# Kernel optimization log

Measured on AMD Instinct MI355X. Metric: run time of the kernel, lower is better.

Reference implementation:

```python
import jax, jax.numpy as jnp
import numpy as np

N, E, G = 64, 128, 4
D0, ED = 9, 4
H1, H2, H3 = 2000, 500, 100
F1, F2, F3 = 1000, 100, 50


def setup_inputs() -> dict:
    key = jax.random.key(0)
    ks = iter(jax.random.split(key, 32))

    def p(shape, s=0.02):
        return (jax.random.normal(next(ks), shape, jnp.float32) * s)

    inp = {
        "x": jax.random.normal(next(ks), (N, D0), jnp.float32),
        "edge_index": jax.random.randint(next(ks), (2, E), 0, N),
        "edge_attr": jax.random.normal(next(ks), (E, ED), jnp.float32),
        "batch": jnp.sort(jax.random.randint(next(ks), (N,), 0, G)),
        # NNConv layer 1: edge MLP Linear(ED, D0*H1), root weight, bias
        "We1": p((ED, D0 * H1)), "be1": p((D0 * H1,)),
        "root1": p((D0, H1)), "b1": p((H1,)),
        # NNConv layer 2
        "We2": p((ED, H1 * H2)), "be2": p((H1 * H2,)),
        "root2": p((H1, H2)), "b2": p((H2,)),
        # NNConv layer 3
        "We3": p((ED, H2 * H3)), "be3": p((H2 * H3,)),
        "root3": p((H2, H3)), "b3": p((H3,)),
        # FCN head
        "W1": p((H3, F1)), "c1": p((F1,)),
        "W2": p((F1, F2)), "c2": p((F2,)),
        "W3": p((F2, F3)), "c3": p((F3,)),
        "W4": p((F3, 1)), "c4": p((1,)),
    }
    return inp


def _nnconv(x, src, dst, edge_attr, We, be, root, b):
    # edge-conditioned weights: [E, in, out]
    in_dim = x.shape[1]
    w = (edge_attr @ We + be).reshape(edge_attr.shape[0], in_dim, -1)
    # gather source feats, per-edge matmul, scatter-add to targets
    msg = jnp.einsum('ei,eio->eo', x[src], w)
    agg = jax.ops.segment_sum(msg, dst, num_segments=x.shape[0])
    return agg + x @ root + b


def reference(x, edge_index, edge_attr, batch,
              We1, be1, root1, b1,
              We2, be2, root2, b2,
              We3, be3, root3, b3,
              W1, c1, W2, c2, W3, c3, W4, c4):
    src, dst = edge_index[0], edge_index[1]
    h = jax.nn.relu(_nnconv(x, src, dst, edge_attr, We1, be1, root1, b1))
    h = jax.nn.relu(_nnconv(h, src, dst, edge_attr, We2, be2, root2, b2))
    h = jax.nn.relu(_nnconv(h, src, dst, edge_attr, We3, be3, root3, b3))
    # sum readout per graph (dropout layers are identity in eval mode)
    g = jax.ops.segment_sum(h, batch, num_segments=G)  # [G, H3]
    g = jax.nn.relu(g @ W1 + c1)
    g = jax.nn.relu(g @ W2 + c2)
    g = jax.nn.relu(g @ W3 + c3)
    out = g @ W4 + c4
    return out.reshape(-1)  # [G]
```

## Files before the change

### kernel.cpp

```cpp
#include <hip/hip_runtime.h>

#define NN 64
#define EE 128
#define GG 4
#define D0 9
#define EDIM 4
#define H1 2000
#define H2 500
#define H3 100
#define FF1 1000
#define FF2 100
#define FF3 50

#define OFF_ACH  0
#define OFF_Y    24576
#define OFF_P1   28032
#define OFF_Q    156032
#define OFF_PART 924032
#define OFF_P2   2524032
#define OFF_PRE3 2556032
#define OFF_F1   2562432
#define OFF_F2   2566432

__device__ __forceinline__ void gl2lds16(const float* g, float* l) {
    __builtin_amdgcn_global_load_lds(
        (const __attribute__((address_space(1))) unsigned int*)g,
        (__attribute__((address_space(3))) unsigned int*)l,
        16, 0, 0);
}

__device__ __forceinline__ float4 ldf4(const float* p) {
    return *(const float4*)p;
}

__device__ __forceinline__ void waitcnt_vm_n(int n) {
    switch (n) {
    case 0: asm volatile("s_waitcnt vmcnt(0)" ::: "memory"); break;
    case 1: asm volatile("s_waitcnt vmcnt(1)" ::: "memory"); break;
    case 2: asm volatile("s_waitcnt vmcnt(2)" ::: "memory"); break;
    case 3: asm volatile("s_waitcnt vmcnt(3)" ::: "memory"); break;
    case 4: asm volatile("s_waitcnt vmcnt(4)" ::: "memory"); break;
    case 5: asm volatile("s_waitcnt vmcnt(5)" ::: "memory"); break;
    default: asm volatile("s_waitcnt vmcnt(6)" ::: "memory"); break;
    }
}
__device__ __forceinline__ void cfence() { asm volatile("" ::: "memory"); }

__global__ __launch_bounds__(256) void k_init(
    const float* __restrict__ x, const int* __restrict__ edge_index,
    const float* __restrict__ edge_attr, const float* __restrict__ c2,
    float* __restrict__ ws)
{
    const int b = blockIdx.x, tid = threadIdx.x;
    if (b == 0) {
        float* A = ws + OFF_ACH;
        for (int i = tid; i < 6 * NN * NN; i += 256) A[i] = 0.f;
        __syncthreads();
        if (tid < EE) {
            int s = edge_index[tid];
            int t = edge_index[EE + tid];
            #pragma unroll
            for (int d = 0; d < 4; ++d)
                atomicAdd(A + d * 4096 + t * 64 + s, edge_attr[tid * 4 + d]);
            atomicAdd(A + 4 * 4096 + t * 64 + s, 1.0f);
        }
        if (tid < NN) A[5 * 4096 + tid * 64 + tid] = 1.0f;
    } else if (b == 1) {
        __shared__ float Ys[NN * 54];
        for (int i = tid; i < NN * 54; i += 256) Ys[i] = 0.f;
        __syncthreads();
        if (tid < EE) {
            int s = edge_index[tid];
            int t = edge_index[EE + tid];
            float ea[4];
            #pragma unroll
            for (int d = 0; d < 4; ++d) ea[d] = edge_attr[tid * 4 + d];
            #pragma unroll
            for (int i = 0; i < D0; ++i) {
                float xv = x[s * D0 + i];
                #pragma unroll
                for (int d = 0; d < 4; ++d)
                    atomicAdd(&Ys[t * 54 + d * 9 + i], ea[d] * xv);
                atomicAdd(&Ys[t * 54 + 36 + i], xv);
            }
        }
        if (tid < NN) {
            #pragma unroll
            for (int i = 0; i < D0; ++i) Ys[tid * 54 + 45 + i] = x[tid * D0 + i];
        }
        __syncthreads();
        for (int i = tid; i < NN * 54; i += 256) ws[OFF_Y + i] = Ys[i];
    } else {
        for (int i = tid; i < GG * FF2; i += 256) ws[OFF_F2 + i] = c2[i % FF2];
    }
}

__global__ __launch_bounds__(256) void k_lin1(
    const float* __restrict__ Yw,
    const float* __restrict__ We1, const float* __restrict__ be1,
    const float* __restrict__ root1, const float* __restrict__ b1,
    float* __restrict__ pre1)
{
    const int tid = threadIdx.x;
    const int tx = tid & 15, ty = tid >> 4;
    const int o0 = blockIdx.x * 64;
    const int w = min(64, H1 - o0);

    __shared__ float Ys[64 * 56];
    __shared__ __align__(16) float Bs[54 * 64];

    for (int i = tid; i < 64 * 54; i += 256) {
        int u = i / 54, r = i - u * 54;
        Ys[u * 56 + r] = Yw[i];
    }
    for (int i = tid; i < 54 * 64; i += 256) {
        int r = i >> 6, c = i & 63;
        int d = r / 9, ii = r - d * 9;
        const float* rowp = ((d < 4) ? (We1 + d * (D0 * H1))
                                     : ((d == 4) ? be1 : root1)) + ii * H1;
        Bs[r * 64 + c] = (c < w) ? rowp[o0 + c] : 0.f;
    }
    __syncthreads();

    float acc[4][4] = {};
    #pragma unroll 6
    for (int r = 0; r < 54; ++r) {
        float a0 = Ys[(ty * 4 + 0) * 56 + r];
        float a1 = Ys[(ty * 4 + 1) * 56 + r];
        float a2 = Ys[(ty * 4 + 2) * 56 + r];
        float a3 = Ys[(ty * 4 + 3) * 56 + r];
        const float4 bv = *(const float4*)&Bs[r * 64 + tx * 4];
        acc[0][0] += a0 * bv.x; acc[0][1] += a0 * bv.y; acc[0][2] += a0 * bv.z; acc[0][3] += a0 * bv.w;
        acc[1][0] += a1 * bv.x; acc[1][1] += a1 * bv.y; acc[1][2] += a1 * bv.z; acc[1][3] += a1 * bv.w;
        acc[2][0] += a2 * bv.x; acc[2][1] += a2 * bv.y; acc[2][2] += a2 * bv.z; acc[2][3] += a2 * bv.w;
        acc[3][0] += a3 * bv.x; acc[3][1] += a3 * bv.y; acc[3][2] += a3 * bv.z; acc[3][3] += a3 * bv.w;
    }
    #pragma unroll
    for (int i = 0; i < 4; ++i) {
        int u = ty * 4 + i;
        #pragma unroll
        for (int jj = 0; jj < 4; ++jj) {
            int j = o0 + tx * 4 + jj;
            if (j < H1) {
                float v = b1[j] + acc[i][jj];
                pre1[u * H1 + j] = v > 0.f ? v : 0.f;
            }
        }
    }
}

template<int Kd, int KTOT, int NKT>
__global__ __launch_bounds__(256) void k_q(
    const float* __restrict__ Ach, const float* __restrict__ P,
    float* __restrict__ Qf)
{
    const int bx = blockIdx.x;
    const int d = bx / NKT, kt = bx % NKT;
    const int k0 = kt * 128;
    const int tid = threadIdx.x;
    const int kq = tid & 31;
    const int rg = tid >> 5;
    const int nf4 = (min(128, Kd - k0) + 3) >> 2;

    __shared__ __align__(16) float Al[64 * 64];
    __shared__ __align__(16) float Pl[64 * 128];

    const float* Ad = Ach + d * 4096;
    for (int i4 = tid; i4 < 1024; i4 += 256)
        *(float4*)&Al[i4 * 4] = ldf4(Ad + i4 * 4);
    for (int i4 = tid; i4 < 64 * 32; i4 += 256) {
        int u = i4 >> 5, c4 = i4 & 31;
        float4 v = {0.f, 0.f, 0.f, 0.f};
        if (c4 < nf4) v = ldf4(P + u * Kd + k0 + c4 * 4);
        *(float4*)&Pl[u * 128 + c4 * 4] = v;
    }
    __syncthreads();

    float acc[8][4] = {};
    #pragma unroll 4
    for (int u4 = 0; u4 < 16; ++u4) {
        float4 pv0 = ldf4(&Pl[(u4 * 4 + 0) * 128 + kq * 4]);
        float4 pv1 = ldf4(&Pl[(u4 * 4 + 1) * 128 + kq * 4]);
        float4 pv2 = ldf4(&Pl[(u4 * 4 + 2) * 128 + kq * 4]);
        float4 pv3 = ldf4(&Pl[(u4 * 4 + 3) * 128 + kq * 4]);
        #pragma unroll
        for (int i = 0; i < 8; ++i) {
            float4 a = ldf4(&Al[(rg * 8 + i) * 64 + u4 * 4]);
            acc[i][0] += a.x * pv0.x + a.y * pv1.x + a.z * pv2.x + a.w * pv3.x;
            acc[i][1] += a.x * pv0.y + a.y * pv1.y + a.z * pv2.y + a.w * pv3.y;
            acc[i][2] += a.x * pv0.z + a.y * pv1.z + a.z * pv2.z + a.w * pv3.z;
            acc[i][3] += a.x * pv0.w + a.y * pv1.w + a.z * pv2.w + a.w * pv3.w;
        }
    }
    const int k = k0 + kq * 4;
    if (k < Kd) {
        #pragma unroll
        for (int i = 0; i < 8; ++i) {
            int r = rg * 8 + i;
            *(float4*)(Qf + r * KTOT + d * Kd + k) =
                make_float4(acc[i][0], acc[i][1], acc[i][2], acc[i][3]);
        }
    }
}

template<int M, int OT, int S, int ITERS, int T1, int T2>
__global__ __launch_bounds__(256) void k_split(
    const float* __restrict__ Qf, const float* __restrict__ We,
    const float* __restrict__ be, const float* __restrict__ root,
    float* __restrict__ part)
{
    constexpr int KC = 20, BN = 32;
    constexpr int KTOT = S * ITERS * KC;
    constexpr int AC = (64 * KC) / 256;
    constexpr int BFL = KC * BN;
    constexpr int BC = (BFL + 255) / 256;
    const int b = blockIdx.x;
    const int s = b % S, ot = b / S;
    const int o0 = ot * BN;
    const int tid = threadIdx.x;
    const int tx = tid & 7, ty = tid >> 3;
    const int wv = tid >> 6, ln = tid & 63;
    const int kbase = s * (KC * ITERS);
    const int nw = ((AC - wv + 3) >> 2) + ((wv < BC) ? ((BC - wv + 3) >> 2) : 0);

    __shared__ __align__(16) float As[2][64 * KC];
    __shared__ __align__(16) float Bs[2][KC * BN];

    auto stage = [&](int bf, int kb) {
        for (int c = wv; c < AC; c += 4) {
            int f = c * 256 + ln * 4;
            int r = f / KC, kkk = f - r * KC;
            gl2lds16(Qf + r * KTOT + kb + kkk, &As[bf][c * 256]);
        }
        for (int c = wv; c < BC; c += 4) {
            int f = c * 256 + ln * 4;
            if (f < BFL) {
                int krow = f / BN, col = f - krow * BN;
                int kg = kb + krow;
                const float* bp = (kg < T1) ? (We + (long long)kg * M)
                                : (kg < T2) ? (be + (long long)(kg - T1) * M)
                                            : (root + (long long)(kg - T2) * M);
                int cc = min(o0 + col, M - 4);
                gl2lds16(bp + cc, &Bs[bf][c * 256]);
            }
        }
    };

    float acc[2][4] = {};
    stage(0, kbase);

    for (int it = 0; it < ITERS; ++it) {
        int npend = 0;
        if (it + 1 < ITERS) { stage((it + 1) & 1, kbase + (it + 1) * KC); npend = nw; }
        waitcnt_vm_n(npend);
        __builtin_amdgcn_s_barrier();
        __builtin_amdgcn_sched_barrier(0);

        const float* Ab = As[it & 1];
        const float* Bb = Bs[it & 1];
        #pragma unroll
        for (int k4 = 0; k4 < KC / 4; ++k4) {
            float4 a0 = ldf4(&Ab[(ty * 2 + 0) * KC + k4 * 4]);
            float4 a1 = ldf4(&Ab[(ty * 2 + 1) * KC + k4 * 4]);
            float4 b0 = ldf4(&Bb[(k4 * 4 + 0) * BN + tx * 4]);
            float4 b1 = ldf4(&Bb[(k4 * 4 + 1) * BN + tx * 4]);
            float4 b2 = ldf4(&Bb[(k4 * 4 + 2) * BN + tx * 4]);
            float4 b3 = ldf4(&Bb[(k4 * 4 + 3) * BN + tx * 4]);
            acc[0][0] += a0.x * b0.x; acc[0][1] += a0.x * b0.y; acc[0][2] += a0.x * b0.z; acc[0][3] += a0.x * b0.w;
            acc[0][0] += a0.y * b1.x; acc[0][1] += a0.y * b1.y; acc[0][2] += a0.y * b1.z; acc[0][3] += a0.y * b1.w;
            acc[0][0] += a0.z * b2.x; acc[0][1] += a0.z * b2.y; acc[0][2] += a0.z * b2.z; acc[0][3] += a0.z * b2.w;
            acc[0][0] += a0.w * b3.x; acc[0][1] += a0.w * b3.y; acc[0][2] += a0.w * b3.z; acc[0][3] += a0.w * b3.w;
            acc[1][0] += a1.x * b0.x; acc[1][1] += a1.x * b0.y; acc[1][2] += a1.x * b0.z; acc[1][3] += a1.x * b0.w;
            acc[1][0] += a1.y * b1.x; acc[1][1] += a1.y * b1.y; acc[1][2] += a1.y * b1.z; acc[1][3] += a1.y * b1.w;
            acc[1][0] += a1.z * b2.x; acc[1][1] += a1.z * b2.y; acc[1][2] += a1.z * b2.z; acc[1][3] += a1.z * b2.w;
            acc[1][0] += a1.w * b3.x; acc[1][1] += a1.w * b3.y; acc[1][2] += a1.w * b3.z; acc[1][3] += a1.w * b3.w;
        }
        cfence();
        __builtin_amdgcn_sched_barrier(0);
        __builtin_amdgcn_s_barrier();
    }

    float* dst = part + s * (64 * M);
    #pragma unroll
    for (int i = 0; i < 2; ++i) {
        int u = ty * 2 + i;
        #pragma unroll
        for (int jj = 0; jj < 4; ++jj) {
            int j = o0 + tx * 4 + jj;
            if (j < M) dst[u * M + j] = acc[i][jj];
        }
    }
}

__global__ __launch_bounds__(256) void k_red2(
    const float* __restrict__ part, const float* __restrict__ b2,
    float* __restrict__ P2)
{
    int i4 = blockIdx.x * 256 + threadIdx.x;
    if (i4 >= (64 * 500) / 4) return;
    int o = (i4 * 4) % 500;
    float4 acc = ldf4(b2 + o);
    #pragma unroll 10
    for (int s = 0; s < 50; ++s) {
        float4 v = ldf4(part + s * 32000 + i4 * 4);
        acc.x += v.x; acc.y += v.y; acc.z += v.z; acc.w += v.w;
    }
    acc.x = fmaxf(acc.x, 0.f); acc.y = fmaxf(acc.y, 0.f);
    acc.z = fmaxf(acc.z, 0.f); acc.w = fmaxf(acc.w, 0.f);
    *(float4*)(P2 + i4 * 4) = acc;
}

__global__ __launch_bounds__(256) void k_red3(
    const float* __restrict__ part, const float* __restrict__ b3,
    float* __restrict__ pre3)
{
    int i4 = blockIdx.x * 256 + threadIdx.x;
    if (i4 >= (64 * 100) / 4) return;
    int o = (i4 * 4) % 100;
    float4 acc = ldf4(b3 + o);
    #pragma unroll 10
    for (int s = 0; s < 50; ++s) {
        float4 v = ldf4(part + s * 6400 + i4 * 4);
        acc.x += v.x; acc.y += v.y; acc.z += v.z; acc.w += v.w;
    }
    *(float4*)(pre3 + i4 * 4) = acc;
}

__global__ __launch_bounds__(256) void k_head1(
    const float* __restrict__ pre3, const int* __restrict__ batch,
    const float* __restrict__ W1, const float* __restrict__ c1,
    float* __restrict__ f1)
{
    const int gi = blockIdx.x >> 4;
    const int jt = blockIdx.x & 15;
    const int o0 = jt * 64;
    const int tid = threadIdx.x;
    __shared__ int   bsh[NN];
    __shared__ float gs[H3];
    __shared__ float red[4 * 64];

    if (tid < NN) bsh[tid] = batch[tid];
    __syncthreads();
    for (int d = tid; d < H3; d += 256) {
        float acc = 0.f;
        #pragma unroll
        for (int v = 0; v < NN; ++v) {
            float h = pre3[v * H3 + d];
            h = h > 0.f ? h : 0.f;
            acc += (bsh[v] == gi) ? h : 0.f;
        }
        gs[d] = acc;
    }
    __syncthreads();
    const int jj = tid & 63, kq = tid >> 6;
    const int oc = min(o0 + jj, FF1 - 1);
    float p = 0.f;
    #pragma unroll
    for (int k = kq * 25; k < kq * 25 + 25; ++k)
        p += gs[k] * W1[k * FF1 + oc];
    red[kq * 64 + jj] = p;
    __syncthreads();
    if (tid < 64) {
        int o = o0 + tid;
        if (o < FF1) {
            float v = c1[o] + red[tid] + red[64 + tid] + red[128 + tid] + red[192 + tid];
            f1[gi * FF1 + o] = v > 0.f ? v : 0.f;
        }
    }
}

__global__ __launch_bounds__(256) void k_head2(
    const float* __restrict__ f1, const float* __restrict__ W2,
    float* __restrict__ f2)
{
    const int s = blockIdx.x;
    const int k0 = s * 63;
    const int kn = min(63, FF1 - k0);
    const int tid = threadIdx.x;
    __shared__ float f1s[4 * 63];
    for (int i = tid; i < 4 * kn; i += 256) {
        int gi = i / kn, kk = i - gi * kn;
        f1s[gi * 63 + kk] = f1[gi * FF1 + k0 + kk];
    }
    __syncthreads();
    for (int idx = tid; idx < GG * FF2; idx += 256) {
        int gi = idx / FF2, o = idx - gi * FF2;
        float acc = 0.f;
        for (int kk = 0; kk < kn; ++kk)
            acc += f1s[gi * 63 + kk] * W2[(k0 + kk) * FF2 + o];
        atomicAdd(&f2[idx], acc);
    }
}

__global__ __launch_bounds__(256) void k_head3(
    const float* __restrict__ f2, const float* __restrict__ W3,
    const float* __restrict__ c3, const float* __restrict__ W4,
    const float* __restrict__ c4, float* __restrict__ out)
{
    const int tid = threadIdx.x;
    __shared__ float f2s[GG * FF2];
    __shared__ float f3s[GG * FF3];
    for (int i = tid; i < GG * FF2; i += 256) {
        float v = f2[i];
        f2s[i] = v > 0.f ? v : 0.f;
    }
    __syncthreads();
    if (tid < GG * FF3) {
        int gi = tid / FF3, o = tid - gi * FF3;
        float acc = c3[o];
        for (int k = 0; k < FF2; ++k)
            acc += f2s[gi * FF2 + k] * W3[k * FF3 + o];
        f3s[tid] = acc > 0.f ? acc : 0.f;
    }
    __syncthreads();
    if (tid < GG) {
        float acc = c4[0];
        #pragma unroll
        for (int k = 0; k < FF3; ++k) acc += f3s[tid * FF3 + k] * W4[k];
        out[tid] = acc;
    }
}

extern "C" void kernel_launch(void* const* d_in, const int* in_sizes, int n_in,
                              void* d_out, int out_size, void* d_ws, size_t ws_size,
                              hipStream_t stream) {
    const float* x          = (const float*)d_in[0];
    const int*   edge_index = (const int*)  d_in[1];
    const float* edge_attr  = (const float*)d_in[2];
    const int*   batch      = (const int*)  d_in[3];
    const float* We1 = (const float*)d_in[4];
    const float* be1 = (const float*)d_in[5];
    const float* root1 = (const float*)d_in[6];
    const float* b1  = (const float*)d_in[7];
    const float* We2 = (const float*)d_in[8];
    const float* be2 = (const float*)d_in[9];
    const float* root2 = (const float*)d_in[10];
    const float* b2  = (const float*)d_in[11];
    const float* We3 = (const float*)d_in[12];
    const float* be3 = (const float*)d_in[13];
    const float* root3 = (const float*)d_in[14];
    const float* b3  = (const float*)d_in[15];
    const float* W1 = (const float*)d_in[16];
    const float* c1 = (const float*)d_in[17];
    const float* W2 = (const float*)d_in[18];
    const float* c2 = (const float*)d_in[19];
    const float* W3 = (const float*)d_in[20];
    const float* c3 = (const float*)d_in[21];
    const float* W4 = (const float*)d_in[22];
    const float* c4 = (const float*)d_in[23];
    float* ws  = (float*)d_ws;
    float* out = (float*)d_out;

    k_init<<<3, 256, 0, stream>>>(x, edge_index, edge_attr, c2, ws);
    k_lin1<<<32, 256, 0, stream>>>(ws + OFF_Y, We1, be1, root1, b1, ws + OFF_P1);
    k_q<2000, 12000, 16><<<96, 256, 0, stream>>>(ws + OFF_ACH, ws + OFF_P1,
                                                 ws + OFF_Q);
    k_split<500, 16, 50, 12, 8000, 10000><<<800, 256, 0, stream>>>(
        ws + OFF_Q, We2, be2, root2, ws + OFF_PART);
    k_red2<<<32, 256, 0, stream>>>(ws + OFF_PART, b2, ws + OFF_P2);
    k_q<500, 3000, 4><<<24, 256, 0, stream>>>(ws + OFF_ACH, ws + OFF_P2,
                                              ws + OFF_Q);
    k_split<100, 4, 50, 3, 2000, 2500><<<200, 256, 0, stream>>>(
        ws + OFF_Q, We3, be3, root3, ws + OFF_PART);
    k_red3<<<7, 256, 0, stream>>>(ws + OFF_PART, b3, ws + OFF_PRE3);
    k_head1<<<64, 256, 0, stream>>>(ws + OFF_PRE3, batch, W1, c1, ws + OFF_F1);
    k_head2<<<16, 256, 0, stream>>>(ws + OFF_F1, W2, ws + OFF_F2);
    k_head3<<<1, 256, 0, stream>>>(ws + OFF_F2, W3, c3, W4, c4, out);
}
```

Baseline: 216.5 us.

## Fuse init/reduction kernels into consumers and widen split GEMM tile

Removes the separate init, red2, red3 and head2/head3 kernels. Each consumer now rebuilds the adjacency matrices in shared memory, sums the split-K partials on load, or computes the FC head tail in a single block, which cuts the launch count from 11 to 7. The split GEMM tile widens from 32 to 64 output columns with a 4x4 per-thread micro-tile, which halves the grid. The cost is redundant recomputation: adjacency building is repeated in every block, the 50-way partial reduction is repeated in each head1 block, and the single-block head2 no longer spreads its work across blocks.

```diff
diff --git a/kernel.cpp b/kernel.cpp
--- a/kernel.cpp
+++ b/kernel.cpp
@@ -4,7 +4,6 @@
 #define EE 128
 #define GG 4
 #define D0 9
-#define EDIM 4
 #define H1 2000
 #define H2 500
 #define H3 100
@@ -12,15 +11,10 @@
 #define FF2 100
 #define FF3 50
 
-#define OFF_ACH  0
-#define OFF_Y    24576
 #define OFF_P1   28032
 #define OFF_Q    156032
 #define OFF_PART 924032
-#define OFF_P2   2524032
-#define OFF_PRE3 2556032
 #define OFF_F1   2562432
-#define OFF_F2   2566432
 
 __device__ __forceinline__ void gl2lds16(const float* g, float* l) {
     __builtin_amdgcn_global_load_lds(
@@ -36,82 +30,93 @@
 __device__ __forceinline__ void waitcnt_vm_n(int n) {
     switch (n) {
     case 0: asm volatile("s_waitcnt vmcnt(0)" ::: "memory"); break;
-    case 1: asm volatile("s_waitcnt vmcnt(1)" ::: "memory"); break;
     case 2: asm volatile("s_waitcnt vmcnt(2)" ::: "memory"); break;
-    case 3: asm volatile("s_waitcnt vmcnt(3)" ::: "memory"); break;
     case 4: asm volatile("s_waitcnt vmcnt(4)" ::: "memory"); break;
-    case 5: asm volatile("s_waitcnt vmcnt(5)" ::: "memory"); break;
     default: asm volatile("s_waitcnt vmcnt(6)" ::: "memory"); break;
     }
 }
 __device__ __forceinline__ void cfence() { asm volatile("" ::: "memory"); }
 
-__global__ __launch_bounds__(256) void k_init(
+__device__ __forceinline__ void build_Ad(float* Al, int d,
+    const int* __restrict__ ei, const float* __restrict__ ea, int tid)
+{
+    for (int i = tid; i < NN * NN; i += 256) Al[i] = 0.f;
+    __syncthreads();
+    if (d == 5) {
+        if (tid < NN) Al[tid * 64 + tid] = 1.0f;
+    } else if (tid < EE) {
+        int s = ei[tid], t = ei[EE + tid];
+        float v = (d < 4) ? ea[tid * 4 + d] : 1.0f;
+        atomicAdd(&Al[t * 64 + s], v);
+    }
+}
+
+template<int Kd, int KTOT>
+__device__ __forceinline__ void q_compute_store(
+    const float* Al, const float* Pl, float* __restrict__ Qf,
+    int d, int k0, int tid)
+{
+    const int kq = tid & 31, rg = tid >> 5;
+    float acc[8][4] = {};
+    #pragma unroll 4
+    for (int u4 = 0; u4 < 16; ++u4) {
+        float4 pv0 = ldf4(&Pl[(u4 * 4 + 0) * 128 + kq * 4]);
+        float4 pv1 = ldf4(&Pl[(u4 * 4 + 1) * 128 + kq * 4]);
+        float4 pv2 = ldf4(&Pl[(u4 * 4 + 2) * 128 + kq * 4]);
+        float4 pv3 = ldf4(&Pl[(u4 * 4 + 3) * 128 + kq * 4]);
+        #pragma unroll
+        for (int i = 0; i < 8; ++i) {
+            float4 a = ldf4(&Al[(rg * 8 + i) * 64 + u4 * 4]);
+            acc[i][0] += a.x * pv0.x + a.y * pv1.x + a.z * pv2.x + a.w * pv3.x;
+            acc[i][1] += a.x * pv0.y + a.y * pv1.y + a.z * pv2.y + a.w * pv3.y;
+            acc[i][2] += a.x * pv0.z + a.y * pv1.z + a.z * pv2.z + a.w * pv3.z;
+            acc[i][3] += a.x * pv0.w + a.y * pv1.w + a.z * pv2.w + a.w * pv3.w;
+        }
+    }
+    const int k = k0 + kq * 4;
+    if (k < Kd) {
+        #pragma unroll
+        for (int i = 0; i < 8; ++i) {
+            int r = rg * 8 + i;
+            *(float4*)(Qf + r * KTOT + d * Kd + k) =
+                make_float4(acc[i][0], acc[i][1], acc[i][2], acc[i][3]);
+        }
+    }
+}
+
+__global__ __launch_bounds__(256) void k_p1(
     const float* __restrict__ x, const int* __restrict__ edge_index,
-    const float* __restrict__ edge_attr, const float* __restrict__ c2,
-    float* __restrict__ ws)
-{
-    const int b = blockIdx.x, tid = threadIdx.x;
-    if (b == 0) {
-        float* A = ws + OFF_ACH;
-        for (int i = tid; i < 6 * NN * NN; i += 256) A[i] = 0.f;
-        __syncthreads();
-        if (tid < EE) {
-            int s = edge_index[tid];
-            int t = edge_index[EE + tid];
-            #pragma unroll
-            for (int d = 0; d < 4; ++d)
-                atomicAdd(A + d * 4096 + t * 64 + s, edge_attr[tid * 4 + d]);
-            atomicAdd(A + 4 * 4096 + t * 64 + s, 1.0f);
-        }
-        if (tid < NN) A[5 * 4096 + tid * 64 + tid] = 1.0f;
-    } else if (b == 1) {
-        __shared__ float Ys[NN * 54];
-        for (int i = tid; i < NN * 54; i += 256) Ys[i] = 0.f;
-        __syncthreads();
-        if (tid < EE) {
-            int s = edge_index[tid];
-            int t = edge_index[EE + tid];
-            float ea[4];
-            #pragma unroll
-            for (int d = 0; d < 4; ++d) ea[d] = edge_attr[tid * 4 + d];
-            #pragma unroll
-            for (int i = 0; i < D0; ++i) {
-                float xv = x[s * D0 + i];
-                #pragma unroll
-                for (int d = 0; d < 4; ++d)
-                    atomicAdd(&Ys[t * 54 + d * 9 + i], ea[d] * xv);
-                atomicAdd(&Ys[t * 54 + 36 + i], xv);
-            }
-        }
-        if (tid < NN) {
-            #pragma unroll
-            for (int i = 0; i < D0; ++i) Ys[tid * 54 + 45 + i] = x[tid * D0 + i];
-        }
-        __syncthreads();
-        for (int i = tid; i < NN * 54; i += 256) ws[OFF_Y + i] = Ys[i];
-    } else {
-        for (int i = tid; i < GG * FF2; i += 256) ws[OFF_F2 + i] = c2[i % FF2];
-    }
-}
-
-__global__ __launch_bounds__(256) void k_lin1(
-    const float* __restrict__ Yw,
+    const float* __restrict__ edge_attr,
     const float* __restrict__ We1, const float* __restrict__ be1,
     const float* __restrict__ root1, const float* __restrict__ b1,
-    float* __restrict__ pre1)
-{
+    float* __restrict__ P1)
+{
+    __shared__ float Ys[64 * 56];
+    __shared__ __align__(16) float Bs[54 * 64];
     const int tid = threadIdx.x;
     const int tx = tid & 15, ty = tid >> 4;
     const int o0 = blockIdx.x * 64;
     const int w = min(64, H1 - o0);
 
-    __shared__ float Ys[64 * 56];
-    __shared__ __align__(16) float Bs[54 * 64];
-
-    for (int i = tid; i < 64 * 54; i += 256) {
-        int u = i / 54, r = i - u * 54;
-        Ys[u * 56 + r] = Yw[i];
+    for (int i = tid; i < 64 * 56; i += 256) Ys[i] = 0.f;
+    __syncthreads();
+    if (tid < EE) {
+        int s = edge_index[tid], t = edge_index[EE + tid];
+        float ea[4];
+        #pragma unroll
+        for (int d = 0; d < 4; ++d) ea[d] = edge_attr[tid * 4 + d];
+        #pragma unroll
+        for (int i = 0; i < D0; ++i) {
+            float xv = x[s * D0 + i];
+            #pragma unroll
+            for (int d = 0; d < 4; ++d)
+                atomicAdd(&Ys[t * 56 + d * 9 + i], ea[d] * xv);
+            atomicAdd(&Ys[t * 56 + 36 + i], xv);
+        }
+    }
+    if (tid < NN) {
+        #pragma unroll
+        for (int i = 0; i < D0; ++i) Ys[tid * 56 + 45 + i] = x[tid * D0 + i];
     }
     for (int i = tid; i < 54 * 64; i += 256) {
         int r = i >> 6, c = i & 63;
@@ -143,112 +148,108 @@
             int j = o0 + tx * 4 + jj;
             if (j < H1) {
                 float v = b1[j] + acc[i][jj];
-                pre1[u * H1 + j] = v > 0.f ? v : 0.f;
+                P1[u * H1 + j] = v > 0.f ? v : 0.f;
             }
         }
     }
 }
 
 template<int Kd, int KTOT, int NKT>
-__global__ __launch_bounds__(256) void k_q(
-    const float* __restrict__ Ach, const float* __restrict__ P,
-    float* __restrict__ Qf)
-{
-    const int bx = blockIdx.x;
-    const int d = bx / NKT, kt = bx % NKT;
-    const int k0 = kt * 128;
-    const int tid = threadIdx.x;
-    const int kq = tid & 31;
-    const int rg = tid >> 5;
-    const int nf4 = (min(128, Kd - k0) + 3) >> 2;
-
+__global__ __launch_bounds__(256) void k_qp(
+    const int* __restrict__ edge_index, const float* __restrict__ edge_attr,
+    const float* __restrict__ P, float* __restrict__ Qf)
+{
     __shared__ __align__(16) float Al[64 * 64];
     __shared__ __align__(16) float Pl[64 * 128];
-
-    const float* Ad = Ach + d * 4096;
-    for (int i4 = tid; i4 < 1024; i4 += 256)
-        *(float4*)&Al[i4 * 4] = ldf4(Ad + i4 * 4);
-    for (int i4 = tid; i4 < 64 * 32; i4 += 256) {
+    const int tid = threadIdx.x;
+    const int d = blockIdx.x / NKT, kt = blockIdx.x % NKT;
+    const int k0 = kt * 128;
+    const int nf4 = (min(128, Kd - k0) + 3) >> 2;
+
+    build_Ad(Al, d, edge_index, edge_attr, tid);
+    for (int i4 = tid; i4 < 2048; i4 += 256) {
         int u = i4 >> 5, c4 = i4 & 31;
         float4 v = {0.f, 0.f, 0.f, 0.f};
         if (c4 < nf4) v = ldf4(P + u * Kd + k0 + c4 * 4);
         *(float4*)&Pl[u * 128 + c4 * 4] = v;
     }
     __syncthreads();
-
-    float acc[8][4] = {};
-    #pragma unroll 4
-    for (int u4 = 0; u4 < 16; ++u4) {
-        float4 pv0 = ldf4(&Pl[(u4 * 4 + 0) * 128 + kq * 4]);
-        float4 pv1 = ldf4(&Pl[(u4 * 4 + 1) * 128 + kq * 4]);
-        float4 pv2 = ldf4(&Pl[(u4 * 4 + 2) * 128 + kq * 4]);
-        float4 pv3 = ldf4(&Pl[(u4 * 4 + 3) * 128 + kq * 4]);
-        #pragma unroll
-        for (int i = 0; i < 8; ++i) {
-            float4 a = ldf4(&Al[(rg * 8 + i) * 64 + u4 * 4]);
-            acc[i][0] += a.x * pv0.x + a.y * pv1.x + a.z * pv2.x + a.w * pv3.x;
-            acc[i][1] += a.x * pv0.y + a.y * pv1.y + a.z * pv2.y + a.w * pv3.y;
-            acc[i][2] += a.x * pv0.z + a.y * pv1.z + a.z * pv2.z + a.w * pv3.z;
-            acc[i][3] += a.x * pv0.w + a.y * pv1.w + a.z * pv2.w + a.w * pv3.w;
-        }
-    }
-    const int k = k0 + kq * 4;
-    if (k < Kd) {
-        #pragma unroll
-        for (int i = 0; i < 8; ++i) {
-            int r = rg * 8 + i;
-            *(float4*)(Qf + r * KTOT + d * Kd + k) =
-                make_float4(acc[i][0], acc[i][1], acc[i][2], acc[i][3]);
-        }
-    }
-}
-
-template<int M, int OT, int S, int ITERS, int T1, int T2>
+    q_compute_store<Kd, KTOT>(Al, Pl, Qf, d, k0, tid);
+}
+
+template<int Kd, int KTOT, int NKT>
+__global__ __launch_bounds__(256) void k_qf(
+    const int* __restrict__ edge_index, const float* __restrict__ edge_attr,
+    const float* __restrict__ part, const float* __restrict__ bias,
+    float* __restrict__ Qf)
+{
+    __shared__ __align__(16) float Al[64 * 64];
+    __shared__ __align__(16) float Pl[64 * 128];
+    const int tid = threadIdx.x;
+    const int d = blockIdx.x / NKT, kt = blockIdx.x % NKT;
+    const int k0 = kt * 128;
+
+    build_Ad(Al, d, edge_index, edge_attr, tid);
+    for (int i4 = tid; i4 < 2048; i4 += 256) {
+        int u = i4 >> 5, c4 = i4 & 31;
+        int k = k0 + c4 * 4;
+        float4 acc = {0.f, 0.f, 0.f, 0.f};
+        if (k < Kd) {
+            acc = ldf4(bias + k);
+            #pragma unroll 10
+            for (int s = 0; s < 50; ++s) {
+                float4 v = ldf4(part + s * (NN * Kd) + u * Kd + k);
+                acc.x += v.x; acc.y += v.y; acc.z += v.z; acc.w += v.w;
+            }
+            acc.x = fmaxf(acc.x, 0.f); acc.y = fmaxf(acc.y, 0.f);
+            acc.z = fmaxf(acc.z, 0.f); acc.w = fmaxf(acc.w, 0.f);
+        }
+        *(float4*)&Pl[u * 128 + c4 * 4] = acc;
+    }
+    __syncthreads();
+    q_compute_store<Kd, KTOT>(Al, Pl, Qf, d, k0, tid);
+}
+
+template<int M, int S, int ITERS, int T1, int T2>
 __global__ __launch_bounds__(256) void k_split(
     const float* __restrict__ Qf, const float* __restrict__ We,
     const float* __restrict__ be, const float* __restrict__ root,
     float* __restrict__ part)
 {
-    constexpr int KC = 20, BN = 32;
+    constexpr int KC = 20, BN = 64;
     constexpr int KTOT = S * ITERS * KC;
-    constexpr int AC = (64 * KC) / 256;
-    constexpr int BFL = KC * BN;
-    constexpr int BC = (BFL + 255) / 256;
     const int b = blockIdx.x;
     const int s = b % S, ot = b / S;
     const int o0 = ot * BN;
     const int tid = threadIdx.x;
-    const int tx = tid & 7, ty = tid >> 3;
+    const int tx = tid & 15, ty = tid >> 4;
     const int wv = tid >> 6, ln = tid & 63;
     const int kbase = s * (KC * ITERS);
-    const int nw = ((AC - wv + 3) >> 2) + ((wv < BC) ? ((BC - wv + 3) >> 2) : 0);
+    const int nw = (wv == 0) ? 4 : 2;
 
     __shared__ __align__(16) float As[2][64 * KC];
     __shared__ __align__(16) float Bs[2][KC * BN];
 
     auto stage = [&](int bf, int kb) {
-        for (int c = wv; c < AC; c += 4) {
+        for (int c = wv; c < 5; c += 4) {
             int f = c * 256 + ln * 4;
             int r = f / KC, kkk = f - r * KC;
             gl2lds16(Qf + r * KTOT + kb + kkk, &As[bf][c * 256]);
         }
-        for (int c = wv; c < BC; c += 4) {
+        for (int c = wv; c < 5; c += 4) {
             int f = c * 256 + ln * 4;
-            if (f < BFL) {
-                int krow = f / BN, col = f - krow * BN;
-                int kg = kb + krow;
-                const float* bp = (kg < T1) ? (We + (long long)kg * M)
-                                : (kg < T2) ? (be + (long long)(kg - T1) * M)
-                                            : (root + (long long)(kg - T2) * M);
-                int cc = min(o0 + col, M - 4);
-                gl2lds16(bp + cc, &Bs[bf][c * 256]);
-            }
+            int krow = f >> 6, col = f & 63;
+            int kg = kb + krow;
+            const float* bp = (kg < T1) ? (We + (long long)kg * M)
+                            : (kg < T2) ? (be + (long long)(kg - T1) * M)
+                                        : (root + (long long)(kg - T2) * M);
+            int cc = min(o0 + col, M - 4);
+            gl2lds16(bp + cc, &Bs[bf][c * 256]);
         }
     };
 
-    float acc[2][4] = {};
+    float acc[4][4] = {};
     stage(0, kbase);
-
     for (int it = 0; it < ITERS; ++it) {
         int npend = 0;
         if (it + 1 < ITERS) { stage((it + 1) & 1, kbase + (it + 1) * KC); npend = nw; }
@@ -259,21 +260,25 @@
         const float* Ab = As[it & 1];
         const float* Bb = Bs[it & 1];
         #pragma unroll
-        for (int k4 = 0; k4 < KC / 4; ++k4) {
-            float4 a0 = ldf4(&Ab[(ty * 2 + 0) * KC + k4 * 4]);
-            float4 a1 = ldf4(&Ab[(ty * 2 + 1) * KC + k4 * 4]);
-            float4 b0 = ldf4(&Bb[(k4 * 4 + 0) * BN + tx * 4]);
-            float4 b1 = ldf4(&Bb[(k4 * 4 + 1) * BN + tx * 4]);
-            float4 b2 = ldf4(&Bb[(k4 * 4 + 2) * BN + tx * 4]);
-            float4 b3 = ldf4(&Bb[(k4 * 4 + 3) * BN + tx * 4]);
-            acc[0][0] += a0.x * b0.x; acc[0][1] += a0.x * b0.y; acc[0][2] += a0.x * b0.z; acc[0][3] += a0.x * b0.w;
-            acc[0][0] += a0.y * b1.x; acc[0][1] += a0.y * b1.y; acc[0][2] += a0.y * b1.z; acc[0][3] += a0.y * b1.w;
-            acc[0][0] += a0.z * b2.x; acc[0][1] += a0.z * b2.y; acc[0][2] += a0.z * b2.z; acc[0][3] += a0.z * b2.w;
-            acc[0][0] += a0.w * b3.x; acc[0][1] += a0.w * b3.y; acc[0][2] += a0.w * b3.z; acc[0][3] += a0.w * b3.w;
-            acc[1][0] += a1.x * b0.x; acc[1][1] += a1.x * b0.y; acc[1][2] += a1.x * b0.z; acc[1][3] += a1.x * b0.w;
-            acc[1][0] += a1.y * b1.x; acc[1][1] += a1.y * b1.y; acc[1][2] += a1.y * b1.z; acc[1][3] += a1.y * b1.w;
-            acc[1][0] += a1.z * b2.x; acc[1][1] += a1.z * b2.y; acc[1][2] += a1.z * b2.z; acc[1][3] += a1.z * b2.w;
-            acc[1][0] += a1.w * b3.x; acc[1][1] += a1.w * b3.y; acc[1][2] += a1.w * b3.z; acc[1][3] += a1.w * b3.w;
+        for (int k4 = 0; k4 < 5; ++k4) {
+            float4 av[4], bv[4];
+            #pragma unroll
+            for (int i = 0; i < 4; ++i)
+                av[i] = ldf4(&Ab[(ty * 4 + i) * KC + k4 * 4]);
+            #pragma unroll
+            for (int q = 0; q < 4; ++q)
+                bv[q] = ldf4(&Bb[(k4 * 4 + q) * BN + tx * 4]);
+            #pragma unroll
+            for (int i = 0; i < 4; ++i) {
+                acc[i][0] += av[i].x * bv[0].x; acc[i][1] += av[i].x * bv[0].y;
+                acc[i][2] += av[i].x * bv[0].z; acc[i][3] += av[i].x * bv[0].w;
+                acc[i][0] += av[i].y * bv[1].x; acc[i][1] += av[i].y * bv[1].y;
+                acc[i][2] += av[i].y * bv[1].z; acc[i][3] += av[i].y * bv[1].w;
+                acc[i][0] += av[i].z * bv[2].x; acc[i][1] += av[i].z * bv[2].y;
+                acc[i][2] += av[i].z * bv[2].z; acc[i][3] += av[i].z * bv[2].w;
+                acc[i][0] += av[i].w * bv[3].x; acc[i][1] += av[i].w * bv[3].y;
+                acc[i][2] += av[i].w * bv[3].z; acc[i][3] += av[i].w * bv[3].w;
+            }
         }
         cfence();
         __builtin_amdgcn_sched_barrier(0);
@@ -282,8 +287,8 @@
 
     float* dst = part + s * (64 * M);
     #pragma unroll
-    for (int i = 0; i < 2; ++i) {
-        int u = ty * 2 + i;
+    for (int i = 0; i < 4; ++i) {
+        int u = ty * 4 + i;
         #pragma unroll
         for (int jj = 0; jj < 4; ++jj) {
             int j = o0 + tx * 4 + jj;
@@ -292,42 +297,9 @@
     }
 }
 
-__global__ __launch_bounds__(256) void k_red2(
-    const float* __restrict__ part, const float* __restrict__ b2,
-    float* __restrict__ P2)
-{
-    int i4 = blockIdx.x * 256 + threadIdx.x;
-    if (i4 >= (64 * 500) / 4) return;
-    int o = (i4 * 4) % 500;
-    float4 acc = ldf4(b2 + o);
-    #pragma unroll 10
-    for (int s = 0; s < 50; ++s) {
-        float4 v = ldf4(part + s * 32000 + i4 * 4);
-        acc.x += v.x; acc.y += v.y; acc.z += v.z; acc.w += v.w;
-    }
-    acc.x = fmaxf(acc.x, 0.f); acc.y = fmaxf(acc.y, 0.f);
-    acc.z = fmaxf(acc.z, 0.f); acc.w = fmaxf(acc.w, 0.f);
-    *(float4*)(P2 + i4 * 4) = acc;
-}
-
-__global__ __launch_bounds__(256) void k_red3(
+__global__ __launch_bounds__(256) void k_head1(
     const float* __restrict__ part, const float* __restrict__ b3,
-    float* __restrict__ pre3)
-{
-    int i4 = blockIdx.x * 256 + threadIdx.x;
-    if (i4 >= (64 * 100) / 4) return;
-    int o = (i4 * 4) % 100;
-    float4 acc = ldf4(b3 + o);
-    #pragma unroll 10
-    for (int s = 0; s < 50; ++s) {
-        float4 v = ldf4(part + s * 6400 + i4 * 4);
-        acc.x += v.x; acc.y += v.y; acc.z += v.z; acc.w += v.w;
-    }
-    *(float4*)(pre3 + i4 * 4) = acc;
-}
-
-__global__ __launch_bounds__(256) void k_head1(
-    const float* __restrict__ pre3, const int* __restrict__ batch,
+    const int* __restrict__ batch,
     const float* __restrict__ W1, const float* __restrict__ c1,
     float* __restrict__ f1)
 {
@@ -335,17 +307,28 @@
     const int jt = blockIdx.x & 15;
     const int o0 = jt * 64;
     const int tid = threadIdx.x;
+    __shared__ __align__(16) float pre3s[NN * H3];
     __shared__ int   bsh[NN];
     __shared__ float gs[H3];
     __shared__ float red[4 * 64];
 
+    for (int i4 = tid; i4 < (NN * H3) / 4; i4 += 256) {
+        int off = i4 * 4;
+        float4 acc = ldf4(b3 + off % H3);
+        #pragma unroll 10
+        for (int s = 0; s < 50; ++s) {
+            float4 v = ldf4(part + s * (NN * H3) + off);
+            acc.x += v.x; acc.y += v.y; acc.z += v.z; acc.w += v.w;
+        }
+        *(float4*)&pre3s[off] = acc;
+    }
     if (tid < NN) bsh[tid] = batch[tid];
     __syncthreads();
     for (int d = tid; d < H3; d += 256) {
         float acc = 0.f;
         #pragma unroll
         for (int v = 0; v < NN; ++v) {
-            float h = pre3[v * H3 + d];
+            float h = pre3s[v * H3 + d];
             h = h > 0.f ? h : 0.f;
             acc += (bsh[v] == gi) ? h : 0.f;
         }
@@ -369,40 +352,25 @@
     }
 }
 
-__global__ __launch_bounds__(256) void k_head2(
+__global__ __launch_bounds__(256) void k_head23(
     const float* __restrict__ f1, const float* __restrict__ W2,
-    float* __restrict__ f2)
-{
-    const int s = blockIdx.x;
-    const int k0 = s * 63;
-    const int kn = min(63, FF1 - k0);
-    const int tid = threadIdx.x;
-    __shared__ float f1s[4 * 63];
-    for (int i = tid; i < 4 * kn; i += 256) {
-        int gi = i / kn, kk = i - gi * kn;
-        f1s[gi * 63 + kk] = f1[gi * FF1 + k0 + kk];
-    }
+    const float* __restrict__ c2, const float* __restrict__ W3,
+    const float* __restrict__ c3, const float* __restrict__ W4,
+    const float* __restrict__ c4, float* __restrict__ out)
+{
+    const int tid = threadIdx.x;
+    __shared__ float f1s[GG * FF1];
+    __shared__ float f2s[GG * FF2];
+    __shared__ float f3s[GG * FF3];
+    for (int i = tid; i < GG * FF1; i += 256) f1s[i] = f1[i];
     __syncthreads();
     for (int idx = tid; idx < GG * FF2; idx += 256) {
         int gi = idx / FF2, o = idx - gi * FF2;
-        float acc = 0.f;
-        for (int kk = 0; kk < kn; ++kk)
-            acc += f1s[gi * 63 + kk] * W2[(k0 + kk) * FF2 + o];
-        atomicAdd(&f2[idx], acc);
-    }
-}
-
-__global__ __launch_bounds__(256) void k_head3(
-    const float* __restrict__ f2, const float* __restrict__ W3,
-    const float* __restrict__ c3, const float* __restrict__ W4,
-    const float* __restrict__ c4, float* __restrict__ out)
-{
-    const int tid = threadIdx.x;
-    __shared__ float f2s[GG * FF2];
-    __shared__ float f3s[GG * FF3];
-    for (int i = tid; i < GG * FF2; i += 256) {
-        float v = f2[i];
-        f2s[i] = v > 0.f ? v : 0.f;
+        float acc = c2[o];
+        #pragma unroll 4
+        for (int k = 0; k < FF1; ++k)
+            acc += f1s[gi * FF1 + k] * W2[k * FF2 + o];
+        f2s[idx] = acc > 0.f ? acc : 0.f;
     }
     __syncthreads();
     if (tid < GG * FF3) {
@@ -451,19 +419,17 @@
     float* ws  = (float*)d_ws;
     float* out = (float*)d_out;
 
-    k_init<<<3, 256, 0, stream>>>(x, edge_index, edge_attr, c2, ws);
-    k_lin1<<<32, 256, 0, stream>>>(ws + OFF_Y, We1, be1, root1, b1, ws + OFF_P1);
-    k_q<2000, 12000, 16><<<96, 256, 0, stream>>>(ws + OFF_ACH, ws + OFF_P1,
-                                                 ws + OFF_Q);
-    k_split<500, 16, 50, 12, 8000, 10000><<<800, 256, 0, stream>>>(
+    k_p1<<<32, 256, 0, stream>>>(x, edge_index, edge_attr,
+                                 We1, be1, root1, b1, ws + OFF_P1);
+    k_qp<2000, 12000, 16><<<96, 256, 0, stream>>>(edge_index, edge_attr,
+                                                  ws + OFF_P1, ws + OFF_Q);
+    k_split<500, 50, 12, 8000, 10000><<<400, 256, 0, stream>>>(
         ws + OFF_Q, We2, be2, root2, ws + OFF_PART);
-    k_red2<<<32, 256, 0, stream>>>(ws + OFF_PART, b2, ws + OFF_P2);
-    k_q<500, 3000, 4><<<24, 256, 0, stream>>>(ws + OFF_ACH, ws + OFF_P2,
-                                              ws + OFF_Q);
-    k_split<100, 4, 50, 3, 2000, 2500><<<200, 256, 0, stream>>>(
+    k_qf<500, 3000, 4><<<24, 256, 0, stream>>>(edge_index, edge_attr,
+                                               ws + OFF_PART, b2, ws + OFF_Q);
+    k_split<100, 50, 3, 2000, 2500><<<100, 256, 0, stream>>>(
         ws + OFF_Q, We3, be3, root3, ws + OFF_PART);
-    k_red3<<<7, 256, 0, stream>>>(ws + OFF_PART, b3, ws + OFF_PRE3);
-    k_head1<<<64, 256, 0, stream>>>(ws + OFF_PRE3, batch, W1, c1, ws + OFF_F1);
-    k_head2<<<16, 256, 0, stream>>>(ws + OFF_F1, W2, ws + OFF_F2);
-    k_head3<<<1, 256, 0, stream>>>(ws + OFF_F2, W3, c3, W4, c4, out);
-}
+    k_head1<<<64, 256, 0, stream>>>(ws + OFF_PART, b3, batch, W1, c1,
+                                    ws + OFF_F1);
+    k_head23<<<1, 256, 0, stream>>>(ws + OFF_F1, W2, c2, W3, c3, W4, c4, out);
+}
```

Result: slower. 335.0 us (+54.7%).
